# Kernel tuning notes

Hardware: AMD Instinct MI355X
Metric: run time of the kernel (lower is better)

Reference implementation:

```python
import jax, jax.numpy as jnp
import numpy as np

G = 2048        # number of graphs in the batch
TURNS = 6       # debate turns (fixed in source)
NPT = 48        # nodes per (graph, turn) segment
NHID = 128      # config.nhid; mode != 'bidirection' -> nlast = nhid
BN_EPS = 1e-5


def setup_inputs() -> dict:
    key = jax.random.key(0)
    k1, k2, k3 = jax.random.split(key, 3)
    N = G * TURNS * NPT
    hp = jax.random.normal(k1, (N, NHID), dtype=jnp.float32)
    idx = jnp.arange(N, dtype=jnp.int32)
    graph_ids = idx // (TURNS * NPT)          # [N] graph membership
    turn_ids = (idx // NPT) % TURNS           # [N] 'ids' node attribute (turn)
    # xavier_normal_ init as in the source
    W1 = jax.random.normal(k2, (NHID // 2, 2 * NHID), dtype=jnp.float32) * np.sqrt(2.0 / (NHID // 2 + 2 * NHID)).astype(np.float32)
    b1 = jnp.zeros((NHID // 2,), dtype=jnp.float32)
    W4 = jax.random.normal(k3, (1, NHID // 2), dtype=jnp.float32) * np.sqrt(2.0 / (1 + NHID // 2)).astype(np.float32)
    b4 = jnp.zeros((1,), dtype=jnp.float32)
    return {
        "hp": hp, "graph_ids": graph_ids, "turn_ids": turn_ids,
        "W1": W1, "b1": b1, "W4": W4, "b4": b4,
        "bn1_gamma": jnp.ones((1,), jnp.float32), "bn1_beta": jnp.zeros((1,), jnp.float32),
        "bn2_gamma": jnp.ones((1,), jnp.float32), "bn2_beta": jnp.zeros((1,), jnp.float32),
    }


def _bn_eval(x, gamma, beta):
    # BatchNorm1d(1) in eval mode: running_mean=0, running_var=1, single channel
    return x * (gamma / jnp.sqrt(1.0 + BN_EPS)) + beta


def reference(hp, graph_ids, turn_ids, W1, b1, W4, b4,
              bn1_gamma, bn1_beta, bn2_gamma, bn2_beta):
    # fused segment readout keyed on (graph, turn) -- replaces the
    # per-graph per-turn unbatch/filter_nodes Python loops
    seg = graph_ids * TURNS + turn_ids                       # [N]
    nseg = G * TURNS
    hmax = jax.ops.segment_max(hp, seg, num_segments=nseg).reshape(G, TURNS, NHID)
    hmin = jax.ops.segment_min(hp, seg, num_segments=nseg).reshape(G, TURNS, NHID)
    # _read_out_loud(op='max') accumulates even turns into s1,
    # _read_out_loud(op='min') accumulates odd turns into s2
    x1 = hmax[:, 0::2, :].sum(axis=1)                        # [G, NHID]
    x2 = hmin[:, 1::2, :].sum(axis=1)                        # [G, NHID]
    x = jnp.concatenate([x1, x2], axis=-1)[:, None, :]       # [G, 1, 2*NHID]
    # MLP head (eval mode: dropout is identity)
    x = _bn_eval(x, bn1_gamma, bn1_beta)
    y = jax.nn.relu(jnp.einsum('gcl,hl->gch', x, W1) + b1)   # [G, 1, NHID//2]
    y = _bn_eval(y, bn2_gamma, bn2_beta)
    out = jnp.einsum('gch,oh->gco', y, W4) + b4              # [G, 1, 1]
    return out.squeeze()                                     # [G]
```

## Files before the change

kernel.cpp:

```cpp
#include <hip/hip_runtime.h>

#define NGRAPH 2048
#define TURNS  6
#define NPT    48
#define NHID   128
#define NC4    (NHID / 4)
#define BN_EPS 1e-5f
#define GPB    2
#define NBLK   (NGRAPH / GPB)

typedef float f32x4 __attribute__((ext_vector_type(4)));

__device__ __forceinline__ f32x4 f4max(f32x4 a, f32x4 b) {
    f32x4 r;
    r.x = fmaxf(a.x, b.x); r.y = fmaxf(a.y, b.y);
    r.z = fmaxf(a.z, b.z); r.w = fmaxf(a.w, b.w);
    return r;
}
__device__ __forceinline__ f32x4 f4min(f32x4 a, f32x4 b) {
    f32x4 r;
    r.x = fminf(a.x, b.x); r.y = fminf(a.y, b.y);
    r.z = fminf(a.z, b.z); r.w = fminf(a.w, b.w);
    return r;
}
__device__ __forceinline__ f32x4 f4shflxor32(f32x4 a) {
    f32x4 r;
    r.x = __shfl_xor(a.x, 32, 64);
    r.y = __shfl_xor(a.y, 32, 64);
    r.z = __shfl_xor(a.z, 32, 64);
    r.w = __shfl_xor(a.w, 32, 64);
    return r;
}

__global__ __launch_bounds__(384, 6) void ggru_readout_mlp(
    const float* __restrict__ hp,
    const float* __restrict__ W1, const float* __restrict__ b1,
    const float* __restrict__ W4, const float* __restrict__ b4,
    const float* __restrict__ bn1_g, const float* __restrict__ bn1_b,
    const float* __restrict__ bn2_g, const float* __restrict__ bn2_b,
    float* __restrict__ out)
{
    __shared__ f32x4 segres[TURNS][NC4];
    __shared__ float xbn[2 * NHID];

    const int tid  = threadIdx.x;
    const int lane = tid & 63;
    const int turn = tid >> 6;

    const float bn1s = bn1_g[0] / sqrtf(1.0f + BN_EPS);
    const float bn1t = bn1_b[0];
    const float bn2s = bn2_g[0] / sqrtf(1.0f + BN_EPS);
    const float bn2t = bn2_b[0];

    #pragma unroll
    for (int gi = 0; gi < GPB; ++gi) {
        const int g = blockIdx.x * GPB + gi;

        const f32x4* base = reinterpret_cast<const f32x4*>(hp)
                          + (size_t)(g * TURNS + turn) * (NPT * NC4) + lane;

        f32x4 a0 = base[0 * 64];
        f32x4 a1 = base[1 * 64];
        f32x4 a2 = base[2 * 64];
        f32x4 a3 = base[3 * 64];
        if ((turn & 1) == 0) {
            #pragma unroll
            for (int c = 4; c < 24; c += 4) {
                a0 = f4max(a0, base[(c + 0) * 64]);
                a1 = f4max(a1, base[(c + 1) * 64]);
                a2 = f4max(a2, base[(c + 2) * 64]);
                a3 = f4max(a3, base[(c + 3) * 64]);
            }
            a0 = f4max(f4max(a0, a1), f4max(a2, a3));
            a0 = f4max(a0, f4shflxor32(a0));
        } else {
            #pragma unroll
            for (int c = 4; c < 24; c += 4) {
                a0 = f4min(a0, base[(c + 0) * 64]);
                a1 = f4min(a1, base[(c + 1) * 64]);
                a2 = f4min(a2, base[(c + 2) * 64]);
                a3 = f4min(a3, base[(c + 3) * 64]);
            }
            a0 = f4min(f4min(a0, a1), f4min(a2, a3));
            a0 = f4min(a0, f4shflxor32(a0));
        }
        if (lane < 32)
            segres[turn][lane] = a0;
        __syncthreads();

        if (tid < 64) {
            const int c = tid & 31;
            f32x4 s;
            if (tid < 32) {
                s = segres[0][c] + segres[2][c] + segres[4][c];
            } else {
                s = segres[1][c] + segres[3][c] + segres[5][c];
            }
            s = s * bn1s;
            s.x += bn1t; s.y += bn1t; s.z += bn1t; s.w += bn1t;
            reinterpret_cast<f32x4*>(xbn)[tid] = s;
        }
        __syncthreads();

        if (tid < 64) {
            float acc2 = b1[tid];
            const f32x4* w  = reinterpret_cast<const f32x4*>(W1 + tid * (2 * NHID));
            const f32x4* xv = reinterpret_cast<const f32x4*>(xbn);
            #pragma unroll 8
            for (int k = 0; k < (2 * NHID) / 4; ++k) {
                const f32x4 wv = w[k];
                const f32x4 x  = xv[k];
                acc2 += wv.x * x.x + wv.y * x.y + wv.z * x.z + wv.w * x.w;
            }
            float y = fmaxf(acc2, 0.0f);
            y = y * bn2s + bn2t;

            float p = y * W4[tid];
            #pragma unroll
            for (int off = 32; off > 0; off >>= 1)
                p += __shfl_down(p, off, 64);
            if (tid == 0)
                out[g] = p + b4[0];
        }
        __syncthreads();
    }
}

extern "C" void kernel_launch(void* const* d_in, const int* in_sizes, int n_in,
                              void* d_out, int out_size, void* d_ws, size_t ws_size,
                              hipStream_t stream) {
    (void)in_sizes; (void)n_in; (void)d_ws; (void)ws_size; (void)out_size;
    const float* hp    = (const float*)d_in[0];
    const float* W1    = (const float*)d_in[3];
    const float* b1    = (const float*)d_in[4];
    const float* W4    = (const float*)d_in[5];
    const float* b4    = (const float*)d_in[6];
    const float* bn1_g = (const float*)d_in[7];
    const float* bn1_b = (const float*)d_in[8];
    const float* bn2_g = (const float*)d_in[9];
    const float* bn2_b = (const float*)d_in[10];
    float* out = (float*)d_out;

    hipLaunchKernelGGL(ggru_readout_mlp, dim3(NBLK), dim3(384), 0, stream,
                       hp, W1, b1, W4, b4, bn1_g, bn1_b, bn2_g, bn2_b, out);
}
```

Before: 68.23 us.

## Split segment reduction and MLP head into two kernels via workspace

Splits the fused kernel into two. The first is a streaming kernel in which each wave reduces one max-turn and one min-turn segment pair and writes the per-segment results to workspace. The second kernel sums the turns and runs the MLP head with one wave per graph. This removes the block-wide syncs and the idle waves during the serial MLP phase, so the memory-bound reduction can stream without stalls. The cost is an extra kernel launch and a small workspace round trip.

```diff
diff --git a/kernel.cpp b/kernel.cpp
--- a/kernel.cpp
+++ b/kernel.cpp
@@ -5,9 +5,11 @@
 #define NPT    48
 #define NHID   128
 #define NC4    (NHID / 4)
+#define PAIR_F4 (NPT * NC4)
 #define BN_EPS 1e-5f
-#define GPB    2
-#define NBLK   (NGRAPH / GPB)
+#define NPAIR  (NGRAPH * TURNS)
+#define ABLK   1536
+#define AWAVES (ABLK * 4)
 
 typedef float f32x4 __attribute__((ext_vector_type(4)));
 
@@ -32,104 +34,103 @@
     return r;
 }
 
-__global__ __launch_bounds__(384, 6) void ggru_readout_mlp(
-    const float* __restrict__ hp,
+__global__ __launch_bounds__(256, 6) void ggru_phase1(
+    const float* __restrict__ hp, float* __restrict__ ws)
+{
+    const int tid  = threadIdx.x;
+    const int lane = tid & 63;
+    const int wv   = (blockIdx.x << 2) | (tid >> 6);
+    const int p0   = wv << 1;
+
+    const f32x4* baseA = reinterpret_cast<const f32x4*>(hp)
+                       + (size_t)p0 * PAIR_F4 + lane;
+    const f32x4* baseB = baseA + PAIR_F4;
+
+    f32x4 a0 = baseA[0 * 64], a1 = baseA[1 * 64],
+          a2 = baseA[2 * 64], a3 = baseA[3 * 64];
+    #pragma unroll
+    for (int c = 4; c < 24; c += 4) {
+        a0 = f4max(a0, baseA[(c + 0) * 64]);
+        a1 = f4max(a1, baseA[(c + 1) * 64]);
+        a2 = f4max(a2, baseA[(c + 2) * 64]);
+        a3 = f4max(a3, baseA[(c + 3) * 64]);
+    }
+    a0 = f4max(f4max(a0, a1), f4max(a2, a3));
+    a0 = f4max(a0, f4shflxor32(a0));
+
+    f32x4 b0 = baseB[0 * 64], b1v = baseB[1 * 64],
+          b2 = baseB[2 * 64], b3 = baseB[3 * 64];
+    #pragma unroll
+    for (int c = 4; c < 24; c += 4) {
+        b0  = f4min(b0,  baseB[(c + 0) * 64]);
+        b1v = f4min(b1v, baseB[(c + 1) * 64]);
+        b2  = f4min(b2,  baseB[(c + 2) * 64]);
+        b3  = f4min(b3,  baseB[(c + 3) * 64]);
+    }
+    b0 = f4min(f4min(b0, b1v), f4min(b2, b3));
+    b0 = f4min(b0, f4shflxor32(b0));
+
+    f32x4* wsv = reinterpret_cast<f32x4*>(ws);
+    if (lane < 32) {
+        wsv[(size_t)p0 * 32 + lane] = a0;
+        wsv[(size_t)(p0 + 1) * 32 + lane] = b0;
+    }
+}
+
+__global__ __launch_bounds__(256) void ggru_phase2(
+    const float* __restrict__ ws,
     const float* __restrict__ W1, const float* __restrict__ b1,
     const float* __restrict__ W4, const float* __restrict__ b4,
     const float* __restrict__ bn1_g, const float* __restrict__ bn1_b,
     const float* __restrict__ bn2_g, const float* __restrict__ bn2_b,
     float* __restrict__ out)
 {
-    __shared__ f32x4 segres[TURNS][NC4];
-    __shared__ float xbn[2 * NHID];
+    __shared__ float xbn[4][2 * NHID];
 
     const int tid  = threadIdx.x;
+    const int wv   = tid >> 6;
     const int lane = tid & 63;
-    const int turn = tid >> 6;
+    const int g    = (blockIdx.x << 2) | wv;
+    const int half = lane >> 5;
+    const int c    = lane & 31;
 
     const float bn1s = bn1_g[0] / sqrtf(1.0f + BN_EPS);
     const float bn1t = bn1_b[0];
     const float bn2s = bn2_g[0] / sqrtf(1.0f + BN_EPS);
     const float bn2t = bn2_b[0];
 
+    const f32x4* wsv = reinterpret_cast<const f32x4*>(ws)
+                     + (size_t)(g * TURNS + half) * 32 + c;
+    f32x4 s = wsv[0] + wsv[2 * 32] + wsv[4 * 32];
+    s = s * bn1s;
+    s.x += bn1t; s.y += bn1t; s.z += bn1t; s.w += bn1t;
+    reinterpret_cast<f32x4*>(xbn[wv])[lane] = s;
+    __syncthreads();
+
+    float acc = b1[lane];
+    const f32x4* wrow = reinterpret_cast<const f32x4*>(W1 + lane * (2 * NHID));
+    const f32x4* xv   = reinterpret_cast<const f32x4*>(xbn[wv]);
+    #pragma unroll 8
+    for (int k = 0; k < (2 * NHID) / 4; ++k) {
+        const f32x4 w = wrow[k];
+        const f32x4 x = xv[k];
+        acc += w.x * x.x + w.y * x.y + w.z * x.z + w.w * x.w;
+    }
+    float y = fmaxf(acc, 0.0f);
+    y = y * bn2s + bn2t;
+
+    float p = y * W4[lane];
     #pragma unroll
-    for (int gi = 0; gi < GPB; ++gi) {
-        const int g = blockIdx.x * GPB + gi;
-
-        const f32x4* base = reinterpret_cast<const f32x4*>(hp)
-                          + (size_t)(g * TURNS + turn) * (NPT * NC4) + lane;
-
-        f32x4 a0 = base[0 * 64];
-        f32x4 a1 = base[1 * 64];
-        f32x4 a2 = base[2 * 64];
-        f32x4 a3 = base[3 * 64];
-        if ((turn & 1) == 0) {
-            #pragma unroll
-            for (int c = 4; c < 24; c += 4) {
-                a0 = f4max(a0, base[(c + 0) * 64]);
-                a1 = f4max(a1, base[(c + 1) * 64]);
-                a2 = f4max(a2, base[(c + 2) * 64]);
-                a3 = f4max(a3, base[(c + 3) * 64]);
-            }
-            a0 = f4max(f4max(a0, a1), f4max(a2, a3));
-            a0 = f4max(a0, f4shflxor32(a0));
-        } else {
-            #pragma unroll
-            for (int c = 4; c < 24; c += 4) {
-                a0 = f4min(a0, base[(c + 0) * 64]);
-                a1 = f4min(a1, base[(c + 1) * 64]);
-                a2 = f4min(a2, base[(c + 2) * 64]);
-                a3 = f4min(a3, base[(c + 3) * 64]);
-            }
-            a0 = f4min(f4min(a0, a1), f4min(a2, a3));
-            a0 = f4min(a0, f4shflxor32(a0));
-        }
-        if (lane < 32)
-            segres[turn][lane] = a0;
-        __syncthreads();
-
-        if (tid < 64) {
-            const int c = tid & 31;
-            f32x4 s;
-            if (tid < 32) {
-                s = segres[0][c] + segres[2][c] + segres[4][c];
-            } else {
-                s = segres[1][c] + segres[3][c] + segres[5][c];
-            }
-            s = s * bn1s;
-            s.x += bn1t; s.y += bn1t; s.z += bn1t; s.w += bn1t;
-            reinterpret_cast<f32x4*>(xbn)[tid] = s;
-        }
-        __syncthreads();
-
-        if (tid < 64) {
-            float acc2 = b1[tid];
-            const f32x4* w  = reinterpret_cast<const f32x4*>(W1 + tid * (2 * NHID));
-            const f32x4* xv = reinterpret_cast<const f32x4*>(xbn);
-            #pragma unroll 8
-            for (int k = 0; k < (2 * NHID) / 4; ++k) {
-                const f32x4 wv = w[k];
-                const f32x4 x  = xv[k];
-                acc2 += wv.x * x.x + wv.y * x.y + wv.z * x.z + wv.w * x.w;
-            }
-            float y = fmaxf(acc2, 0.0f);
-            y = y * bn2s + bn2t;
-
-            float p = y * W4[tid];
-            #pragma unroll
-            for (int off = 32; off > 0; off >>= 1)
-                p += __shfl_down(p, off, 64);
-            if (tid == 0)
-                out[g] = p + b4[0];
-        }
-        __syncthreads();
-    }
+    for (int off = 32; off > 0; off >>= 1)
+        p += __shfl_down(p, off, 64);
+    if (lane == 0)
+        out[g] = p + b4[0];
 }
 
 extern "C" void kernel_launch(void* const* d_in, const int* in_sizes, int n_in,
                               void* d_out, int out_size, void* d_ws, size_t ws_size,
                               hipStream_t stream) {
-    (void)in_sizes; (void)n_in; (void)d_ws; (void)ws_size; (void)out_size;
+    (void)in_sizes; (void)n_in; (void)ws_size; (void)out_size;
     const float* hp    = (const float*)d_in[0];
     const float* W1    = (const float*)d_in[3];
     const float* b1    = (const float*)d_in[4];
@@ -140,7 +141,9 @@
     const float* bn2_g = (const float*)d_in[9];
     const float* bn2_b = (const float*)d_in[10];
     float* out = (float*)d_out;
+    float* ws  = (float*)d_ws;
 
-    hipLaunchKernelGGL(ggru_readout_mlp, dim3(NBLK), dim3(384), 0, stream,
-                       hp, W1, b1, W4, b4, bn1_g, bn1_b, bn2_g, bn2_b, out);
+    hipLaunchKernelGGL(ggru_phase1, dim3(ABLK), dim3(256), 0, stream, hp, ws);
+    hipLaunchKernelGGL(ggru_phase2, dim3(NGRAPH / 4), dim3(256), 0, stream,
+                       ws, W1, b1, W4, b4, bn1_g, bn1_b, bn2_g, bn2_b, out);
 }
```

After: 68.86 us. Within noise of the previous version (+0.9%).
